# Kernel tuning notes

Hardware: AMD Instinct MI355X
Metric: run time of the kernel (lower is better)

Reference implementation:

```python
import jax, jax.numpy as jnp
import numpy as np

B, S, D, H, E, K = 4, 2048, 768, 3072, 8, 2
LB_SCALE = 0.01
NOISY_STD = 1.0


def setup_inputs() -> dict:
    key = jax.random.key(0)
    ks = jax.random.split(key, 8)
    x = jax.random.normal(ks[0], (B, S, D), jnp.float32)
    # gate_linear: nn.Linear(D, E, bias=False); torch weight is [E, D]
    gate_w = jax.random.normal(ks[1], (E, D), jnp.float32) * 0.02
    noise_weight = jnp.zeros((E,), jnp.float32)  # initialized to zeros in torch
    noise = jax.random.normal(ks[2], (B, S, E), jnp.float32)  # torch.randn_like(logits)
    # expert weights stored in (in, out) layout: y = x @ w + b
    w1 = jax.random.normal(ks[3], (E, D, H), jnp.float32) * 0.02
    b1 = jnp.zeros((E, H), jnp.float32)
    w2 = jax.random.normal(ks[4], (E, D, H), jnp.float32) * 0.02
    b2 = jnp.zeros((E, H), jnp.float32)
    wp = jax.random.normal(ks[5], (E, H, D), jnp.float32) * 0.02
    bp = jnp.zeros((E, D), jnp.float32)
    return {"x": x, "gate_w": gate_w, "noise_weight": noise_weight, "noise": noise,
            "w1": w1, "b1": b1, "w2": w2, "b2": b2, "wp": wp, "bp": bp}


def reference(x, gate_w, noise_weight, noise, w1, b1, w2, b2, wp, bp):
    num_experts = gate_w.shape[0]
    # --- TopKGateParallel ---
    logits = jnp.einsum('bsd,ed->bse', x, gate_w)            # [B,S,E]
    gate_weights = jax.nn.softmax(logits, axis=-1)
    gate_weights_mean = gate_weights.reshape(-1, num_experts).mean(0)
    uniform = 1.0 / num_experts
    load_balance_loss = jnp.mean((gate_weights_mean - uniform) ** 2) * LB_SCALE
    logits_noisy = logits + noise * NOISY_STD * noise_weight  # noise_weight zeros => no-op at init
    top_k_vals, top_k_ids = jax.lax.top_k(logits_noisy, K)    # [B,S,K]
    # scatter top-k back into a -inf tensor, then softmax -> sparse gates
    topk_mask = jax.nn.one_hot(top_k_ids, num_experts, dtype=logits.dtype).sum(-2) > 0  # [B,S,E]
    sparse_logits = jnp.where(topk_mask, logits_noisy, -jnp.inf)
    gates = jax.nn.softmax(sparse_logits, axis=-1)            # zeros outside top-k
    # --- per-expert SwiGLU, weighted combine (gates are exactly 0 off top-k) ---
    y = jnp.zeros_like(x)
    for e in range(num_experts):  # small fixed expert count
        h = (x @ w1[e] + b1[e]) * jax.nn.silu(x @ w2[e] + b2[e])  # [B,S,H]
        y = y + gates[..., e:e + 1] * (h @ wp[e] + bp[e])
    return y, load_balance_loss
```

## Files before the change

kernel.cpp:

```cpp
#include <hip/hip_runtime.h>
#include <hip/hip_bf16.h>

#define NTOK 8192
#define DDIM 768
#define HDIM 3072
#define NEXP 8
#define MROWS (NTOK*2)

typedef float f32x4 __attribute__((ext_vector_type(4)));
typedef short bf16x8 __attribute__((ext_vector_type(8)));
typedef unsigned short u16x4 __attribute__((ext_vector_type(4)));

__device__ __forceinline__ unsigned short f2bf(float f) {
  union { float f; unsigned u; } v; v.f = f;
  unsigned r = v.u + 0x7fffu + ((v.u >> 16) & 1u);
  return (unsigned short)(r >> 16);
}

typedef __attribute__((address_space(3))) unsigned int* lds_ptr_t;
typedef const __attribute__((address_space(1))) unsigned int* gbl_ptr_t;
__device__ __forceinline__ void async16(const void* g, void* l) {
  __builtin_amdgcn_global_load_lds((gbl_ptr_t)g, (lds_ptr_t)l, 16, 0, 0);
}

__global__ __launch_bounds__(128) void gating_kernel(
    const float* __restrict__ x, const float* __restrict__ gw,
    const float* __restrict__ nw, const float* __restrict__ noise,
    int* counts, float* sums, int* tok_list, float* gate_list,
    int* tok_top, float* gate_top)
{
  __shared__ float s_gw[NEXP*DDIM];
  __shared__ float s_sums[NEXP];
  __shared__ float s_nw[NEXP];
  int tid = threadIdx.x;
  for (int i = tid; i < NEXP*DDIM/4; i += 128)
    ((f32x4*)s_gw)[i] = ((const f32x4*)gw)[i];
  if (tid < NEXP) { s_sums[tid] = 0.f; s_nw[tid] = nw[tid]; }
  __syncthreads();
  int t = blockIdx.x*128 + tid;
  float acc[NEXP];
  #pragma unroll
  for (int e = 0; e < NEXP; ++e) acc[e] = 0.f;
  const f32x4* xr = (const f32x4*)(x + (size_t)t*DDIM);
  for (int d4 = 0; d4 < DDIM/4; ++d4) {
    f32x4 xv = xr[d4];
    #pragma unroll
    for (int e = 0; e < NEXP; ++e) {
      f32x4 g = *(const f32x4*)&s_gw[e*DDIM + d4*4];
      acc[e] += xv.x*g.x + xv.y*g.y + xv.z*g.z + xv.w*g.w;
    }
  }
  float m = acc[0];
  #pragma unroll
  for (int e = 1; e < NEXP; ++e) m = fmaxf(m, acc[e]);
  float p[NEXP], s = 0.f;
  #pragma unroll
  for (int e = 0; e < NEXP; ++e) { p[e] = __expf(acc[e]-m); s += p[e]; }
  float inv = 1.f/s;
  #pragma unroll
  for (int e = 0; e < NEXP; ++e) atomicAdd(&s_sums[e], p[e]*inv);
  float ln[NEXP];
  #pragma unroll
  for (int e = 0; e < NEXP; ++e) ln[e] = acc[e] + noise[(size_t)t*NEXP+e]*s_nw[e];
  int i0 = 0; float v0 = ln[0];
  #pragma unroll
  for (int e = 1; e < NEXP; ++e) if (ln[e] > v0) { v0 = ln[e]; i0 = e; }
  int i1 = -1; float v1 = 0.f;
  #pragma unroll
  for (int e = 0; e < NEXP; ++e)
    if (e != i0 && (i1 < 0 || ln[e] > v1)) { v1 = ln[e]; i1 = e; }
  float e1 = __expf(v1 - v0);
  float g0 = 1.f/(1.f + e1);
  float g1 = e1*g0;
  int p0 = atomicAdd(&counts[i0], 1);
  tok_list[i0*NTOK + p0] = t; gate_list[i0*NTOK + p0] = g0;
  int p1 = atomicAdd(&counts[i1], 1);
  tok_list[i1*NTOK + p1] = t; gate_list[i1*NTOK + p1] = g1;
  tok_top[2*t] = i0; tok_top[2*t+1] = i1;
  gate_top[2*t] = g0; gate_top[2*t+1] = g1;
  __syncthreads();
  if (tid < NEXP) atomicAdd(&sums[tid], s_sums[tid]);
}

__global__ void finalize_kernel(const int* counts, const float* sums,
                                int* offsets, float* loss_out)
{
  if (threadIdx.x == 0) {
    int o = 0;
    #pragma unroll
    for (int e = 0; e < NEXP; ++e) { offsets[e] = o; o += counts[e]; }
    offsets[NEXP] = o;
    float l = 0.f;
    #pragma unroll
    for (int e = 0; e < NEXP; ++e) {
      float dv = sums[e]*(1.f/(float)NTOK) - 1.f/(float)NEXP;
      l += dv*dv;
    }
    loss_out[0] = l*(0.01f/(float)NEXP);
  }
}

__global__ __launch_bounds__(256) void cvt_x_kernel(const float* __restrict__ x,
                                                    unsigned short* __restrict__ xb)
{
  int i = blockIdx.x*256 + threadIdx.x;
  f32x4 v = ((const f32x4*)x)[i];
  u16x4 o; o.x = f2bf(v.x); o.y = f2bf(v.y); o.z = f2bf(v.z); o.w = f2bf(v.w);
  ((u16x4*)xb)[i] = o;
}

__global__ __launch_bounds__(256) void transpose_cvt_kernel(
    const float* __restrict__ src, unsigned short* __restrict__ dst, int R, int C)
{
  __shared__ unsigned short s[64*65];
  int e = blockIdx.z;
  int r0 = blockIdx.y*64, c0 = blockIdx.x*64;
  const float* sp = src + ((size_t)e*R + r0)*C + c0;
  unsigned short* dp = dst + ((size_t)e*C + c0)*R + r0;
  int t = threadIdx.x;
  #pragma unroll
  for (int i = 0; i < 16; ++i) {
    int idx = t + 256*i;
    int r = idx >> 6, c = idx & 63;
    s[c*65 + r] = f2bf(sp[(size_t)r*C + c]);
  }
  __syncthreads();
  #pragma unroll
  for (int i = 0; i < 16; ++i) {
    int idx = t + 256*i;
    int c = idx >> 6, r = idx & 63;
    dp[(size_t)c*R + r] = s[c*65 + r];
  }
}

__global__ __launch_bounds__(256) void compact_kernel(
    const int* __restrict__ counts, const int* __restrict__ offsets,
    const int* __restrict__ tok_list, const float* __restrict__ gate_list,
    int* __restrict__ row_token, float* __restrict__ row_gate)
{
  int e = blockIdx.y;
  int pos = blockIdx.x*256 + threadIdx.x;
  if (pos < counts[e]) {
    int r = offsets[e] + pos;
    row_token[r] = tok_list[e*NTOK + pos];
    row_gate[r]  = gate_list[e*NTOK + pos];
  }
}

__global__ __launch_bounds__(256) void init_y_kernel(
    const int* __restrict__ tok_top, const float* __restrict__ gate_top,
    const float* __restrict__ bp, float* __restrict__ y)
{
  int i = blockIdx.x*256 + threadIdx.x;
  int t = i / (DDIM/4);
  int d4 = i % (DDIM/4);
  int e0 = tok_top[2*t], e1 = tok_top[2*t+1];
  float g0 = gate_top[2*t], g1 = gate_top[2*t+1];
  f32x4 b0 = ((const f32x4*)(bp + (size_t)e0*DDIM))[d4];
  f32x4 b1v = ((const f32x4*)(bp + (size_t)e1*DDIM))[d4];
  ((f32x4*)y)[i] = g0*b0 + g1*b1v;
}

__global__ __launch_bounds__(256) void ffn1_mfma(
    const unsigned short* __restrict__ xb,
    const unsigned short* __restrict__ w1T, const unsigned short* __restrict__ w2T,
    const float* __restrict__ b1, const float* __restrict__ b2,
    const int* __restrict__ offsets, const int* __restrict__ row_token,
    unsigned short* __restrict__ h_buf, int h_base, int HC)
{
  int e = blockIdx.z;
  int r_lo = offsets[e];
  int rows_e = offsets[e+1] - r_lo;
  int bx = blockIdx.x;
  if (bx*128 >= rows_e) return;
  int r0 = r_lo + bx*128;
  int rows_valid = rows_e - bx*128; if (rows_valid > 128) rows_valid = 128;
  int h0 = h_base + blockIdx.y*64;

  __shared__ __align__(16) char sL[16384];
  __shared__ int s_tok[128];

  int tid = threadIdx.x;
  if (tid < 128) {
    int r = r0 + tid; if (r > MROWS-1) r = MROWS-1;
    s_tok[tid] = row_token[r];
  }
  __syncthreads();
  int lane = tid & 63, wc = tid >> 6;
  int l4r = lane >> 2, l4c = lane & 3;
  int quad = lane >> 4, l16 = lane & 15;

  const unsigned short* gA0 = xb + (size_t)s_tok[wc*16 + l4r]*DDIM + l4c*8;
  const unsigned short* gA1 = xb + (size_t)s_tok[(wc+4)*16 + l4r]*DDIM + l4c*8;
  const unsigned short* gB1 = w1T + ((size_t)e*HDIM + h0 + wc*16 + l4r)*DDIM + l4c*8;
  const unsigned short* gB2 = w2T + ((size_t)e*HDIM + h0 + wc*16 + l4r)*DDIM + l4c*8;
  char* lA0 = sL + wc*1024;
  char* lA1 = sL + (wc+4)*1024;
  char* lB1 = sL + 8192 + wc*1024;
  char* lB2 = sL + 12288 + wc*1024;

  f32x4 acc1[8], acc2[8];
  #pragma unroll
  for (int i = 0; i < 8; ++i) { acc1[i] = (f32x4){0,0,0,0}; acc2[i] = (f32x4){0,0,0,0}; }

  for (int k0 = 0; k0 < DDIM; k0 += 32) {
    async16(gA0 + k0, lA0);
    async16(gA1 + k0, lA1);
    async16(gB1 + k0, lB1);
    async16(gB2 + k0, lB2);
    __syncthreads();
    bf16x8 bf1 = *(const bf16x8*)(sL + 8192 + (wc*16 + l16)*64 + quad*16);
    bf16x8 bf2 = *(const bf16x8*)(sL + 12288 + (wc*16 + l16)*64 + quad*16);
    #pragma unroll
    for (int mt = 0; mt < 8; ++mt) {
      bf16x8 af = *(const bf16x8*)(sL + (mt*16 + l16)*64 + quad*16);
      acc1[mt] = __builtin_amdgcn_mfma_f32_16x16x32_bf16(af, bf1, acc1[mt], 0, 0, 0);
      acc2[mt] = __builtin_amdgcn_mfma_f32_16x16x32_bf16(af, bf2, acc2[mt], 0, 0, 0);
    }
    __syncthreads();
  }
  int hcol = h0 + wc*16 + l16;
  float bb1 = b1[(size_t)e*HDIM + hcol];
  float bb2 = b2[(size_t)e*HDIM + hcol];
  int hl = hcol - h_base;
  #pragma unroll
  for (int mt = 0; mt < 8; ++mt) {
    #pragma unroll
    for (int r = 0; r < 4; ++r) {
      int row = mt*16 + quad*4 + r;
      if (row < rows_valid) {
        float c1 = acc1[mt][r] + bb1;
        float c2 = acc2[mt][r] + bb2;
        float hv = c1 * (c2 / (1.f + __expf(-c2)));
        h_buf[(size_t)(r0 + row)*HC + hl] = f2bf(hv);
      }
    }
  }
}

__global__ __launch_bounds__(256) void ffn2_mfma(
    const unsigned short* __restrict__ h_buf, const unsigned short* __restrict__ wpT,
    const int* __restrict__ offsets, const int* __restrict__ row_token,
    const float* __restrict__ row_gate, float* __restrict__ y, int h_base, int HC)
{
  int e = blockIdx.z;
  int r_lo = offsets[e];
  int rows_e = offsets[e+1] - r_lo;
  int bx = blockIdx.x;
  if (bx*128 >= rows_e) return;
  int r0 = r_lo + bx*128;
  int rows_valid = rows_e - bx*128; if (rows_valid > 128) rows_valid = 128;
  int c0 = blockIdx.y*128;

  __shared__ __align__(16) char sL[16384];
  __shared__ int s_tok[128];
  __shared__ float s_gate[128];

  int tid = threadIdx.x;
  if (tid < 128) {
    int r = r0 + tid; if (r > MROWS-1) r = MROWS-1;
    s_tok[tid]  = row_token[r];
    s_gate[tid] = row_gate[r];
  }
  int lane = tid & 63, wc = tid >> 6;
  int l4r = lane >> 2, l4c = lane & 3;
  int quad = lane >> 4, l16 = lane & 15;

  int rA0 = r0 + wc*16 + l4r;     if (rA0 > MROWS-1) rA0 = MROWS-1;
  int rA1 = r0 + (wc+4)*16 + l4r; if (rA1 > MROWS-1) rA1 = MROWS-1;
  const unsigned short* gA0 = h_buf + (size_t)rA0*HC + l4c*8;
  const unsigned short* gA1 = h_buf + (size_t)rA1*HC + l4c*8;
  const unsigned short* gB0 = wpT + ((size_t)e*DDIM + c0 + wc*16 + l4r)*HDIM + h_base + l4c*8;
  const unsigned short* gB1 = wpT + ((size_t)e*DDIM + c0 + (wc+4)*16 + l4r)*HDIM + h_base + l4c*8;
  char* lA0 = sL + wc*1024;
  char* lA1 = sL + (wc+4)*1024;
  char* lB0 = sL + 8192 + wc*1024;
  char* lB1 = sL + 8192 + (wc+4)*1024;

  f32x4 acc[8][2];
  #pragma unroll
  for (int i = 0; i < 8; ++i) { acc[i][0] = (f32x4){0,0,0,0}; acc[i][1] = (f32x4){0,0,0,0}; }
  __syncthreads();

  for (int k0 = 0; k0 < HC; k0 += 32) {
    async16(gA0 + k0, lA0);
    async16(gA1 + k0, lA1);
    async16(gB0 + k0, lB0);
    async16(gB1 + k0, lB1);
    __syncthreads();
    bf16x8 bfr0 = *(const bf16x8*)(sL + 8192 + (wc*32 + l16)*64 + quad*16);
    bf16x8 bfr1 = *(const bf16x8*)(sL + 8192 + (wc*32 + 16 + l16)*64 + quad*16);
    #pragma unroll
    for (int mt = 0; mt < 8; ++mt) {
      bf16x8 af = *(const bf16x8*)(sL + (mt*16 + l16)*64 + quad*16);
      acc[mt][0] = __builtin_amdgcn_mfma_f32_16x16x32_bf16(af, bfr0, acc[mt][0], 0, 0, 0);
      acc[mt][1] = __builtin_amdgcn_mfma_f32_16x16x32_bf16(af, bfr1, acc[mt][1], 0, 0, 0);
    }
    __syncthreads();
  }
  #pragma unroll
  for (int nt = 0; nt < 2; ++nt) {
    int col = c0 + wc*32 + nt*16 + l16;
    #pragma unroll
    for (int mt = 0; mt < 8; ++mt) {
      #pragma unroll
      for (int r = 0; r < 4; ++r) {
        int row = mt*16 + quad*4 + r;
        if (row < rows_valid)
          atomicAdd(&y[(size_t)s_tok[row]*DDIM + col], s_gate[row]*acc[mt][nt][r]);
      }
    }
  }
}

__global__ __launch_bounds__(256) void ffn2_kernel(
    const unsigned short* __restrict__ h_buf, const float* __restrict__ wp,
    const int* __restrict__ offsets, const int* __restrict__ row_token,
    const float* __restrict__ row_gate, float* __restrict__ y, int h_base, int HC)
{
  int e = blockIdx.z;
  int r_lo = offsets[e];
  int rows_e = offsets[e+1] - r_lo;
  int bx = blockIdx.x;
  if (bx*128 >= rows_e) return;
  int r0 = r_lo + bx*128;
  int rows_valid = rows_e - bx*128; if (rows_valid > 128) rows_valid = 128;
  int c0 = blockIdx.y*128;

  __shared__ unsigned short sA[128*40];
  __shared__ int s_tok[128];
  __shared__ float s_gate[128];

  int tid = threadIdx.x;
  if (tid < 128) {
    int r = r0 + tid; if (r > MROWS-1) r = MROWS-1;
    s_tok[tid]  = row_token[r];
    s_gate[tid] = row_gate[r];
  }
  int lane = tid & 63;
  int wc = tid >> 6;
  int quad = lane >> 4, l16 = lane & 15;

  const float* wp0 = wp + (size_t)e*HDIM*DDIM + c0 + wc*32 + l16;

  f32x4 acc[8][2];
  #pragma unroll
  for (int i = 0; i < 8; ++i) { acc[i][0] = (f32x4){0,0,0,0}; acc[i][1] = (f32x4){0,0,0,0}; }
  __syncthreads();

  for (int k0 = 0; k0 < HC; k0 += 32) {
    #pragma unroll
    for (int i = 0; i < 2; ++i) {
      int c = i*256 + tid;
      int row = c >> 2, k8 = c & 3;
      int rr = r0 + row; if (rr > MROWS-1) rr = MROWS-1;
      bf16x8 v = *(const bf16x8*)(h_buf + (size_t)rr*HC + k0 + k8*8);
      *(bf16x8*)&sA[row*40 + k8*8] = v;
    }
    float bv[2][8];
    #pragma unroll
    for (int nt = 0; nt < 2; ++nt)
      #pragma unroll
      for (int j = 0; j < 8; ++j)
        bv[nt][j] = wp0[(size_t)(h_base + k0 + quad*8 + j)*DDIM + nt*16];
    bf16x8 bfr[2];
    #pragma unroll
    for (int nt = 0; nt < 2; ++nt)
      #pragma unroll
      for (int j = 0; j < 8; ++j) bfr[nt][j] = (short)f2bf(bv[nt][j]);
    __syncthreads();
    #pragma unroll
    for (int mt = 0; mt < 8; ++mt) {
      bf16x8 af = *(const bf16x8*)&sA[(mt*16 + l16)*40 + quad*8];
      acc[mt][0] = __builtin_amdgcn_mfma_f32_16x16x32_bf16(af, bfr[0], acc[mt][0], 0, 0, 0);
      acc[mt][1] = __builtin_amdgcn_mfma_f32_16x16x32_bf16(af, bfr[1], acc[mt][1], 0, 0, 0);
    }
    __syncthreads();
  }
  #pragma unroll
  for (int nt = 0; nt < 2; ++nt) {
    int col = c0 + wc*32 + nt*16 + l16;
    #pragma unroll
    for (int mt = 0; mt < 8; ++mt) {
      #pragma unroll
      for (int r = 0; r < 4; ++r) {
        int row = mt*16 + quad*4 + r;
        if (row < rows_valid)
          atomicAdd(&y[(size_t)s_tok[row]*DDIM + col], s_gate[row]*acc[mt][nt][r]);
      }
    }
  }
}

extern "C" void kernel_launch(void* const* d_in, const int* in_sizes, int n_in,
                              void* d_out, int out_size, void* d_ws, size_t ws_size,
                              hipStream_t stream)
{
  (void)in_sizes; (void)n_in; (void)out_size;
  const float* x     = (const float*)d_in[0];
  const float* gw    = (const float*)d_in[1];
  const float* nw    = (const float*)d_in[2];
  const float* noise = (const float*)d_in[3];
  const float* w1    = (const float*)d_in[4];
  const float* b1    = (const float*)d_in[5];
  const float* w2    = (const float*)d_in[6];
  const float* b2    = (const float*)d_in[7];
  const float* wp    = (const float*)d_in[8];
  const float* bp    = (const float*)d_in[9];
  float* y = (float*)d_out;

  char* ws = (char*)d_ws;
  int*   counts   = (int*)(ws + 0);
  float* sums     = (float*)(ws + 64);
  int*   offsets  = (int*)(ws + 128);
  size_t off = 256;
  int*   tok_list  = (int*)(ws + off);   off += (size_t)NEXP*NTOK*4;
  float* gate_list = (float*)(ws + off); off += (size_t)NEXP*NTOK*4;
  int*   tok_top   = (int*)(ws + off);   off += (size_t)NTOK*2*4;
  float* gate_top  = (float*)(ws + off); off += (size_t)NTOK*2*4;
  int*   row_token = (int*)(ws + off);   off += (size_t)MROWS*4;
  float* row_gate  = (float*)(ws + off); off += (size_t)MROWS*4;
  unsigned short* xb = (unsigned short*)(ws + off); off += (size_t)NTOK*DDIM*2;

  const size_t WT = (size_t)NEXP*DDIM*HDIM*2;
  unsigned short* w1T = (unsigned short*)(ws + off);
  unsigned short* w2T = (unsigned short*)(ws + off + WT);
  unsigned short* wpT = (unsigned short*)(ws + off + 2*WT);
  bool haveP = (off + 3*WT + (size_t)MROWS*64*2 <= ws_size);
  size_t oH = off + (haveP ? 3*WT : 2*WT);

  static const int hc_opts[6] = {3072, 1536, 768, 384, 192, 64};
  int HC = 64;
  for (int i = 0; i < 6; ++i)
    if (oH + (size_t)MROWS*hc_opts[i]*2 <= ws_size) { HC = hc_opts[i]; break; }
  unsigned short* h_buf = (unsigned short*)(ws + oH);

  hipMemsetAsync(d_ws, 0, 256, stream);
  gating_kernel<<<NTOK/128, 128, 0, stream>>>(x, gw, nw, noise, counts, sums,
                                              tok_list, gate_list, tok_top, gate_top);
  finalize_kernel<<<1, 64, 0, stream>>>(counts, sums, offsets, y + (size_t)NTOK*DDIM);
  cvt_x_kernel<<<NTOK*DDIM/1024, 256, 0, stream>>>(x, xb);
  compact_kernel<<<dim3(NTOK/256, NEXP), 256, 0, stream>>>(counts, offsets, tok_list,
                                                           gate_list, row_token, row_gate);
  init_y_kernel<<<NTOK*DDIM/1024, 256, 0, stream>>>(tok_top, gate_top, bp, y);

  transpose_cvt_kernel<<<dim3(HDIM/64, DDIM/64, NEXP), 256, 0, stream>>>(w1, w1T, DDIM, HDIM);
  transpose_cvt_kernel<<<dim3(HDIM/64, DDIM/64, NEXP), 256, 0, stream>>>(w2, w2T, DDIM, HDIM);
  if (haveP)
    transpose_cvt_kernel<<<dim3(DDIM/64, HDIM/64, NEXP), 256, 0, stream>>>(wp, wpT, HDIM, DDIM);

  int nch = HDIM / HC;
  for (int c = 0; c < nch; ++c) {
    ffn1_mfma<<<dim3(64, HC/64, NEXP), 256, 0, stream>>>(xb, w1T, w2T, b1, b2, offsets,
                                                         row_token, h_buf, c*HC, HC);
    if (haveP)
      ffn2_mfma<<<dim3(64, DDIM/128, NEXP), 256, 0, stream>>>(h_buf, wpT, offsets, row_token,
                                                              row_gate, y, c*HC, HC);
    else
      ffn2_kernel<<<dim3(64, DDIM/128, NEXP), 256, 0, stream>>>(h_buf, wp, offsets, row_token,
                                                                row_gate, y, c*HC, HC);
  }
}
```

Baseline: 999.3 us.

## Enlarge MoE GEMM tiles and XOR-swizzle LDS layout in ffn1/ffn2

ffn1 now uses 512-thread blocks computing 256x128 tiles for both w1 and w2, and ffn2 computes 256x128 tiles with 4x8 MFMA subtiles per wave. This raises MFMA work per LDS load and cuts redundant reloads of the weight and activation tiles. The LDS layout is XOR-swizzled on the 16-byte k segment to reduce bank conflicts on fragment reads. The minimum h chunk size and the grids are adjusted to match. The trade-offs are more registers per thread, fewer blocks when few tokens are routed to an expert, and more padding waste on ragged tiles.

Result: slower. 1.725 ms (+72.6%).

```diff
diff --git a/kernel.cpp b/kernel.cpp
--- a/kernel.cpp
+++ b/kernel.cpp
@@ -161,7 +161,7 @@
   ((f32x4*)y)[i] = g0*b0 + g1*b1v;
 }
 
-__global__ __launch_bounds__(256) void ffn1_mfma(
+__global__ __launch_bounds__(512, 2) void ffn1_mfma(
     const unsigned short* __restrict__ xb,
     const unsigned short* __restrict__ w1T, const unsigned short* __restrict__ w2T,
     const float* __restrict__ b1, const float* __restrict__ b2,
@@ -172,36 +172,46 @@
   int r_lo = offsets[e];
   int rows_e = offsets[e+1] - r_lo;
   int bx = blockIdx.x;
-  if (bx*128 >= rows_e) return;
-  int r0 = r_lo + bx*128;
-  int rows_valid = rows_e - bx*128; if (rows_valid > 128) rows_valid = 128;
-  int h0 = h_base + blockIdx.y*64;
-
-  __shared__ __align__(16) char sL[16384];
-  __shared__ int s_tok[128];
+  if (bx*256 >= rows_e) return;
+  int r0 = r_lo + bx*256;
+  int rows_valid = rows_e - bx*256; if (rows_valid > 256) rows_valid = 256;
+  int h0 = h_base + blockIdx.y*128;
+
+  __shared__ __align__(16) char sA[16384];
+  __shared__ __align__(16) char sB[16384];
+  __shared__ int s_tok[256];
 
   int tid = threadIdx.x;
-  if (tid < 128) {
+  if (tid < 256) {
     int r = r0 + tid; if (r > MROWS-1) r = MROWS-1;
     s_tok[tid] = row_token[r];
   }
   __syncthreads();
-  int lane = tid & 63, wc = tid >> 6;
-  int l4r = lane >> 2, l4c = lane & 3;
-  int quad = lane >> 4, l16 = lane & 15;
-
-  const unsigned short* gA0 = xb + (size_t)s_tok[wc*16 + l4r]*DDIM + l4c*8;
-  const unsigned short* gA1 = xb + (size_t)s_tok[(wc+4)*16 + l4r]*DDIM + l4c*8;
-  const unsigned short* gB1 = w1T + ((size_t)e*HDIM + h0 + wc*16 + l4r)*DDIM + l4c*8;
-  const unsigned short* gB2 = w2T + ((size_t)e*HDIM + h0 + wc*16 + l4r)*DDIM + l4c*8;
-  char* lA0 = sL + wc*1024;
-  char* lA1 = sL + (wc+4)*1024;
-  char* lB1 = sL + 8192 + wc*1024;
-  char* lB2 = sL + 12288 + wc*1024;
-
-  f32x4 acc1[8], acc2[8];
-  #pragma unroll
-  for (int i = 0; i < 8; ++i) { acc1[i] = (f32x4){0,0,0,0}; acc2[i] = (f32x4){0,0,0,0}; }
+
+  int lane = tid & 63, w = tid >> 6;
+  int wr = w & 3, wcg = w >> 2;
+  int l16 = lane & 15, quad = lane >> 4;
+  int lr = lane >> 2, ls = lane & 3;
+  int kseg = ls ^ (lr & 3);
+
+  const unsigned short* gA0 = xb + (size_t)s_tok[w*16 + lr]*DDIM + kseg*8;
+  const unsigned short* gA1 = xb + (size_t)s_tok[(8+w)*16 + lr]*DDIM + kseg*8;
+  const unsigned short* gB1 = w1T + ((size_t)e*HDIM + h0 + w*16 + lr)*DDIM + kseg*8;
+  const unsigned short* gB2 = w2T + ((size_t)e*HDIM + h0 + w*16 + lr)*DDIM + kseg*8;
+  char* lA0 = sA + w*1024;
+  char* lA1 = sA + (8+w)*1024;
+  char* lB1 = sB + w*1024;
+  char* lB2 = sB + (8+w)*1024;
+
+  f32x4 acc[2][4][4];
+  #pragma unroll
+  for (int m = 0; m < 2; ++m)
+    #pragma unroll
+    for (int i = 0; i < 4; ++i)
+      #pragma unroll
+      for (int j = 0; j < 4; ++j) acc[m][i][j] = (f32x4){0,0,0,0};
+
+  int swz = (quad ^ (l16 & 3))*16 + l16*64;
 
   for (int k0 = 0; k0 < DDIM; k0 += 32) {
     async16(gA0 + k0, lA0);
@@ -209,36 +219,46 @@
     async16(gB1 + k0, lB1);
     async16(gB2 + k0, lB2);
     __syncthreads();
-    bf16x8 bf1 = *(const bf16x8*)(sL + 8192 + (wc*16 + l16)*64 + quad*16);
-    bf16x8 bf2 = *(const bf16x8*)(sL + 12288 + (wc*16 + l16)*64 + quad*16);
-    #pragma unroll
-    for (int mt = 0; mt < 8; ++mt) {
-      bf16x8 af = *(const bf16x8*)(sL + (mt*16 + l16)*64 + quad*16);
-      acc1[mt] = __builtin_amdgcn_mfma_f32_16x16x32_bf16(af, bf1, acc1[mt], 0, 0, 0);
-      acc2[mt] = __builtin_amdgcn_mfma_f32_16x16x32_bf16(af, bf2, acc2[mt], 0, 0, 0);
-    }
-    __syncthreads();
-  }
-  int hcol = h0 + wc*16 + l16;
-  float bb1 = b1[(size_t)e*HDIM + hcol];
-  float bb2 = b2[(size_t)e*HDIM + hcol];
-  int hl = hcol - h_base;
-  #pragma unroll
-  for (int mt = 0; mt < 8; ++mt) {
-    #pragma unroll
-    for (int r = 0; r < 4; ++r) {
-      int row = mt*16 + quad*4 + r;
-      if (row < rows_valid) {
-        float c1 = acc1[mt][r] + bb1;
-        float c2 = acc2[mt][r] + bb2;
-        float hv = c1 * (c2 / (1.f + __expf(-c2)));
-        h_buf[(size_t)(r0 + row)*HC + hl] = f2bf(hv);
+    bf16x8 bfr[2][4];
+    #pragma unroll
+    for (int m = 0; m < 2; ++m)
+      #pragma unroll
+      for (int nt = 0; nt < 4; ++nt)
+        bfr[m][nt] = *(const bf16x8*)(sB + (m*8 + wcg*4 + nt)*1024 + swz);
+    #pragma unroll
+    for (int mt = 0; mt < 4; ++mt) {
+      bf16x8 af = *(const bf16x8*)(sA + (wr*4 + mt)*1024 + swz);
+      #pragma unroll
+      for (int m = 0; m < 2; ++m)
+        #pragma unroll
+        for (int nt = 0; nt < 4; ++nt)
+          acc[m][mt][nt] = __builtin_amdgcn_mfma_f32_16x16x32_bf16(af, bfr[m][nt], acc[m][mt][nt], 0, 0, 0);
+    }
+    __syncthreads();
+  }
+  #pragma unroll
+  for (int nt = 0; nt < 4; ++nt) {
+    int col = h0 + wcg*64 + nt*16 + l16;
+    float bb1 = b1[(size_t)e*HDIM + col];
+    float bb2 = b2[(size_t)e*HDIM + col];
+    int cl = col - h_base;
+    #pragma unroll
+    for (int mt = 0; mt < 4; ++mt) {
+      #pragma unroll
+      for (int r = 0; r < 4; ++r) {
+        int row = wr*64 + mt*16 + quad*4 + r;
+        if (row < rows_valid) {
+          float c1 = acc[0][mt][nt][r] + bb1;
+          float c2 = acc[1][mt][nt][r] + bb2;
+          float hv = c1 * (c2 / (1.f + __expf(-c2)));
+          h_buf[(size_t)(r0 + row)*HC + cl] = f2bf(hv);
+        }
       }
     }
   }
 }
 
-__global__ __launch_bounds__(256) void ffn2_mfma(
+__global__ __launch_bounds__(256, 2) void ffn2_mfma(
     const unsigned short* __restrict__ h_buf, const unsigned short* __restrict__ wpT,
     const int* __restrict__ offsets, const int* __restrict__ row_token,
     const float* __restrict__ row_gate, float* __restrict__ y, int h_base, int HC)
@@ -247,65 +267,75 @@
   int r_lo = offsets[e];
   int rows_e = offsets[e+1] - r_lo;
   int bx = blockIdx.x;
-  if (bx*128 >= rows_e) return;
-  int r0 = r_lo + bx*128;
-  int rows_valid = rows_e - bx*128; if (rows_valid > 128) rows_valid = 128;
+  if (bx*256 >= rows_e) return;
+  int r0 = r_lo + bx*256;
+  int rows_valid = rows_e - bx*256; if (rows_valid > 256) rows_valid = 256;
   int c0 = blockIdx.y*128;
 
-  __shared__ __align__(16) char sL[16384];
-  __shared__ int s_tok[128];
-  __shared__ float s_gate[128];
+  __shared__ __align__(16) char sA[16384];
+  __shared__ __align__(16) char sB[8192];
+  __shared__ int s_tok[256];
+  __shared__ float s_gate[256];
 
   int tid = threadIdx.x;
-  if (tid < 128) {
+  {
     int r = r0 + tid; if (r > MROWS-1) r = MROWS-1;
     s_tok[tid]  = row_token[r];
     s_gate[tid] = row_gate[r];
   }
-  int lane = tid & 63, wc = tid >> 6;
-  int l4r = lane >> 2, l4c = lane & 3;
-  int quad = lane >> 4, l16 = lane & 15;
-
-  int rA0 = r0 + wc*16 + l4r;     if (rA0 > MROWS-1) rA0 = MROWS-1;
-  int rA1 = r0 + (wc+4)*16 + l4r; if (rA1 > MROWS-1) rA1 = MROWS-1;
-  const unsigned short* gA0 = h_buf + (size_t)rA0*HC + l4c*8;
-  const unsigned short* gA1 = h_buf + (size_t)rA1*HC + l4c*8;
-  const unsigned short* gB0 = wpT + ((size_t)e*DDIM + c0 + wc*16 + l4r)*HDIM + h_base + l4c*8;
-  const unsigned short* gB1 = wpT + ((size_t)e*DDIM + c0 + (wc+4)*16 + l4r)*HDIM + h_base + l4c*8;
-  char* lA0 = sL + wc*1024;
-  char* lA1 = sL + (wc+4)*1024;
-  char* lB0 = sL + 8192 + wc*1024;
-  char* lB1 = sL + 8192 + (wc+4)*1024;
-
-  f32x4 acc[8][2];
-  #pragma unroll
-  for (int i = 0; i < 8; ++i) { acc[i][0] = (f32x4){0,0,0,0}; acc[i][1] = (f32x4){0,0,0,0}; }
-  __syncthreads();
+  __syncthreads();
+
+  int lane = tid & 63, w = tid >> 6;
+  int l16 = lane & 15, quad = lane >> 4;
+  int lr = lane >> 2, ls = lane & 3;
+  int kseg = ls ^ (lr & 3);
+
+  const unsigned short* gA[4];
+  #pragma unroll
+  for (int i = 0; i < 4; ++i) {
+    int rr = r0 + (i*4 + w)*16 + lr; if (rr > MROWS-1) rr = MROWS-1;
+    gA[i] = h_buf + (size_t)rr*HC + kseg*8;
+  }
+  const unsigned short* gB[2];
+  #pragma unroll
+  for (int i = 0; i < 2; ++i)
+    gB[i] = wpT + ((size_t)e*DDIM + c0 + (i*4 + w)*16 + lr)*HDIM + h_base + kseg*8;
+
+  f32x4 acc[4][8];
+  #pragma unroll
+  for (int i = 0; i < 4; ++i)
+    #pragma unroll
+    for (int j = 0; j < 8; ++j) acc[i][j] = (f32x4){0,0,0,0};
+
+  int swz = (quad ^ (l16 & 3))*16 + l16*64;
 
   for (int k0 = 0; k0 < HC; k0 += 32) {
-    async16(gA0 + k0, lA0);
-    async16(gA1 + k0, lA1);
-    async16(gB0 + k0, lB0);
-    async16(gB1 + k0, lB1);
-    __syncthreads();
-    bf16x8 bfr0 = *(const bf16x8*)(sL + 8192 + (wc*32 + l16)*64 + quad*16);
-    bf16x8 bfr1 = *(const bf16x8*)(sL + 8192 + (wc*32 + 16 + l16)*64 + quad*16);
-    #pragma unroll
-    for (int mt = 0; mt < 8; ++mt) {
-      bf16x8 af = *(const bf16x8*)(sL + (mt*16 + l16)*64 + quad*16);
-      acc[mt][0] = __builtin_amdgcn_mfma_f32_16x16x32_bf16(af, bfr0, acc[mt][0], 0, 0, 0);
-      acc[mt][1] = __builtin_amdgcn_mfma_f32_16x16x32_bf16(af, bfr1, acc[mt][1], 0, 0, 0);
-    }
-    __syncthreads();
-  }
-  #pragma unroll
-  for (int nt = 0; nt < 2; ++nt) {
-    int col = c0 + wc*32 + nt*16 + l16;
-    #pragma unroll
-    for (int mt = 0; mt < 8; ++mt) {
+    #pragma unroll
+    for (int i = 0; i < 4; ++i) async16(gA[i] + k0, sA + ((i*4 + w)*1024) + 0*(size_t)lane);
+    #pragma unroll
+    for (int i = 0; i < 2; ++i) async16(gB[i] + k0, sB + ((i*4 + w)*1024));
+    __syncthreads();
+    bf16x8 bfr[8];
+    #pragma unroll
+    for (int nt = 0; nt < 8; ++nt)
+      bfr[nt] = *(const bf16x8*)(sB + nt*1024 + swz);
+    #pragma unroll
+    for (int mt = 0; mt < 4; ++mt) {
+      bf16x8 af = *(const bf16x8*)(sA + (w*4 + mt)*1024 + swz);
+      #pragma unroll
+      for (int nt = 0; nt < 8; ++nt)
+        acc[mt][nt] = __builtin_amdgcn_mfma_f32_16x16x32_bf16(af, bfr[nt], acc[mt][nt], 0, 0, 0);
+    }
+    __syncthreads();
+  }
+  #pragma unroll
+  for (int nt = 0; nt < 8; ++nt) {
+    int col = c0 + nt*16 + l16;
+    #pragma unroll
+    for (int mt = 0; mt < 4; ++mt) {
       #pragma unroll
       for (int r = 0; r < 4; ++r) {
-        int row = mt*16 + quad*4 + r;
+        int row = w*64 + mt*16 + quad*4 + r;
         if (row < rows_valid)
           atomicAdd(&y[(size_t)s_tok[row]*DDIM + col], s_gate[row]*acc[mt][nt][r]);
       }
@@ -426,11 +456,11 @@
   unsigned short* w1T = (unsigned short*)(ws + off);
   unsigned short* w2T = (unsigned short*)(ws + off + WT);
   unsigned short* wpT = (unsigned short*)(ws + off + 2*WT);
-  bool haveP = (off + 3*WT + (size_t)MROWS*64*2 <= ws_size);
+  bool haveP = (off + 3*WT + (size_t)MROWS*128*2 <= ws_size);
   size_t oH = off + (haveP ? 3*WT : 2*WT);
 
-  static const int hc_opts[6] = {3072, 1536, 768, 384, 192, 64};
-  int HC = 64;
+  static const int hc_opts[6] = {3072, 1536, 768, 384, 256, 128};
+  int HC = 128;
   for (int i = 0; i < 6; ++i)
     if (oH + (size_t)MROWS*hc_opts[i]*2 <= ws_size) { HC = hc_opts[i]; break; }
   unsigned short* h_buf = (unsigned short*)(ws + oH);
@@ -451,10 +481,10 @@
 
   int nch = HDIM / HC;
   for (int c = 0; c < nch; ++c) {
-    ffn1_mfma<<<dim3(64, HC/64, NEXP), 256, 0, stream>>>(xb, w1T, w2T, b1, b2, offsets,
-                                                         row_token, h_buf, c*HC, HC);
+    ffn1_mfma<<<dim3(32, HC/128, NEXP), 512, 0, stream>>>(xb, w1T, w2T, b1, b2, offsets,
+                                                          row_token, h_buf, c*HC, HC);
     if (haveP)
-      ffn2_mfma<<<dim3(64, DDIM/128, NEXP), 256, 0, stream>>>(h_buf, wpT, offsets, row_token,
+      ffn2_mfma<<<dim3(32, DDIM/128, NEXP), 256, 0, stream>>>(h_buf, wpT, offsets, row_token,
                                                               row_gate, y, c*HC, HC);
     else
       ffn2_kernel<<<dim3(64, DDIM/128, NEXP), 256, 0, stream>>>(h_buf, wp, offsets, row_token,
```

## Deepen MFMA K-tiles, square ffn2 warp tiles, replace atomic combine with gather pass

Applied to the files above, without the earlier changes.

Both expert GEMM kernels now stage 64-wide K slices per barrier instead of 32, which halves the number of sync rounds. ffn2 switches to a 2x2 warp layout with 4x4 accumulator tiles so each warp reuses its A and B fragments more. When the workspace is large enough, the full hidden buffer is computed in one pass. ffn2 then writes per-row partial outputs, and a new combine kernel gathers the two expert results per token with gates and biases, which avoids float atomics into y. Other changes: the w1/w2 transposes are merged into one launch and the grid x dimension is doubled. These cost extra workspace and one more full read and write of the partial buffer.

After: 1.006 ms. No clear change (+0.7%).

```diff
diff --git a/kernel.cpp b/kernel.cpp
--- a/kernel.cpp
+++ b/kernel.cpp
@@ -27,7 +27,7 @@
     const float* __restrict__ x, const float* __restrict__ gw,
     const float* __restrict__ nw, const float* __restrict__ noise,
     int* counts, float* sums, int* tok_list, float* gate_list,
-    int* tok_top, float* gate_top)
+    int* tok_top, float* gate_top, int* pos_top)
 {
   __shared__ float s_gw[NEXP*DDIM];
   __shared__ float s_sums[NEXP];
@@ -78,6 +78,7 @@
   tok_list[i1*NTOK + p1] = t; gate_list[i1*NTOK + p1] = g1;
   tok_top[2*t] = i0; tok_top[2*t+1] = i1;
   gate_top[2*t] = g0; gate_top[2*t+1] = g1;
+  pos_top[2*t] = p0; pos_top[2*t+1] = p1;
   __syncthreads();
   if (tid < NEXP) atomicAdd(&sums[tid], s_sums[tid]);
 }
@@ -107,6 +108,35 @@
   f32x4 v = ((const f32x4*)x)[i];
   u16x4 o; o.x = f2bf(v.x); o.y = f2bf(v.y); o.z = f2bf(v.z); o.w = f2bf(v.w);
   ((u16x4*)xb)[i] = o;
+}
+
+__global__ __launch_bounds__(256) void transpose_cvt2_kernel(
+    const float* __restrict__ src1, unsigned short* __restrict__ dst1,
+    const float* __restrict__ src2, unsigned short* __restrict__ dst2,
+    int R, int C)
+{
+  __shared__ unsigned short s[64*65];
+  int z = blockIdx.z;
+  int e = z & (NEXP-1);
+  const float* src = (z < NEXP) ? src1 : src2;
+  unsigned short* dst = (z < NEXP) ? dst1 : dst2;
+  int r0 = blockIdx.y*64, c0 = blockIdx.x*64;
+  const float* sp = src + ((size_t)e*R + r0)*C + c0;
+  unsigned short* dp = dst + ((size_t)e*C + c0)*R + r0;
+  int t = threadIdx.x;
+  #pragma unroll
+  for (int i = 0; i < 16; ++i) {
+    int idx = t + 256*i;
+    int r = idx >> 6, c = idx & 63;
+    s[c*65 + r] = f2bf(sp[(size_t)r*C + c]);
+  }
+  __syncthreads();
+  #pragma unroll
+  for (int i = 0; i < 16; ++i) {
+    int idx = t + 256*i;
+    int c = idx >> 6, r = idx & 63;
+    dp[(size_t)c*R + r] = s[c*65 + r];
+  }
 }
 
 __global__ __launch_bounds__(256) void transpose_cvt_kernel(
@@ -177,7 +207,8 @@
   int rows_valid = rows_e - bx*128; if (rows_valid > 128) rows_valid = 128;
   int h0 = h_base + blockIdx.y*64;
 
-  __shared__ __align__(16) char sL[16384];
+  __shared__ __align__(16) char sA[16384];
+  __shared__ __align__(16) char sB[16384];
   __shared__ int s_tok[128];
 
   int tid = threadIdx.x;
@@ -186,40 +217,52 @@
     s_tok[tid] = row_token[r];
   }
   __syncthreads();
-  int lane = tid & 63, wc = tid >> 6;
-  int l4r = lane >> 2, l4c = lane & 3;
-  int quad = lane >> 4, l16 = lane & 15;
-
-  const unsigned short* gA0 = xb + (size_t)s_tok[wc*16 + l4r]*DDIM + l4c*8;
-  const unsigned short* gA1 = xb + (size_t)s_tok[(wc+4)*16 + l4r]*DDIM + l4c*8;
-  const unsigned short* gB1 = w1T + ((size_t)e*HDIM + h0 + wc*16 + l4r)*DDIM + l4c*8;
-  const unsigned short* gB2 = w2T + ((size_t)e*HDIM + h0 + wc*16 + l4r)*DDIM + l4c*8;
-  char* lA0 = sL + wc*1024;
-  char* lA1 = sL + (wc+4)*1024;
-  char* lB1 = sL + 8192 + wc*1024;
-  char* lB2 = sL + 12288 + wc*1024;
+
+  int lane = tid & 63, w = tid >> 6;
+  int l16 = lane & 15, quad = lane >> 4;
+  int lr = lane >> 2, ls = lane & 3;
+
+  const unsigned short* gA[4]; char* lA[4];
+  const unsigned short* gB[4]; char* lB[4];
+  #pragma unroll
+  for (int i = 0; i < 4; ++i) {
+    int slot = i*4 + w;
+    int chunk = slot & 7, kh = slot >> 3;
+    gA[i] = xb + (size_t)s_tok[chunk*16 + lr]*DDIM + kh*32 + ls*8;
+    lA[i] = sA + slot*1024;
+    int mat = (slot >> 2) & 1;
+    int col = h0 + w*16 + lr;
+    const unsigned short* base = mat ? w2T : w1T;
+    gB[i] = base + ((size_t)e*HDIM + col)*DDIM + kh*32 + ls*8;
+    lB[i] = sB + slot*1024;
+  }
 
   f32x4 acc1[8], acc2[8];
   #pragma unroll
   for (int i = 0; i < 8; ++i) { acc1[i] = (f32x4){0,0,0,0}; acc2[i] = (f32x4){0,0,0,0}; }
 
-  for (int k0 = 0; k0 < DDIM; k0 += 32) {
-    async16(gA0 + k0, lA0);
-    async16(gA1 + k0, lA1);
-    async16(gB1 + k0, lB1);
-    async16(gB2 + k0, lB2);
+  int fro = l16*64 + quad*16;
+
+  for (int k0 = 0; k0 < DDIM; k0 += 64) {
+    #pragma unroll
+    for (int i = 0; i < 4; ++i) async16(gA[i] + k0, lA[i]);
+    #pragma unroll
+    for (int i = 0; i < 4; ++i) async16(gB[i] + k0, lB[i]);
     __syncthreads();
-    bf16x8 bf1 = *(const bf16x8*)(sL + 8192 + (wc*16 + l16)*64 + quad*16);
-    bf16x8 bf2 = *(const bf16x8*)(sL + 12288 + (wc*16 + l16)*64 + quad*16);
-    #pragma unroll
-    for (int mt = 0; mt < 8; ++mt) {
-      bf16x8 af = *(const bf16x8*)(sL + (mt*16 + l16)*64 + quad*16);
-      acc1[mt] = __builtin_amdgcn_mfma_f32_16x16x32_bf16(af, bf1, acc1[mt], 0, 0, 0);
-      acc2[mt] = __builtin_amdgcn_mfma_f32_16x16x32_bf16(af, bf2, acc2[mt], 0, 0, 0);
+    #pragma unroll
+    for (int kh = 0; kh < 2; ++kh) {
+      bf16x8 bf1 = *(const bf16x8*)(sB + (kh*8 + w)*1024 + fro);
+      bf16x8 bf2 = *(const bf16x8*)(sB + (kh*8 + 4 + w)*1024 + fro);
+      #pragma unroll
+      for (int mt = 0; mt < 8; ++mt) {
+        bf16x8 af = *(const bf16x8*)(sA + (kh*8 + mt)*1024 + fro);
+        acc1[mt] = __builtin_amdgcn_mfma_f32_16x16x32_bf16(af, bf1, acc1[mt], 0, 0, 0);
+        acc2[mt] = __builtin_amdgcn_mfma_f32_16x16x32_bf16(af, bf2, acc2[mt], 0, 0, 0);
+      }
     }
     __syncthreads();
   }
-  int hcol = h0 + wc*16 + l16;
+  int hcol = h0 + w*16 + l16;
   float bb1 = b1[(size_t)e*HDIM + hcol];
   float bb2 = b2[(size_t)e*HDIM + hcol];
   int hl = hcol - h_base;
@@ -241,7 +284,8 @@
 __global__ __launch_bounds__(256) void ffn2_mfma(
     const unsigned short* __restrict__ h_buf, const unsigned short* __restrict__ wpT,
     const int* __restrict__ offsets, const int* __restrict__ row_token,
-    const float* __restrict__ row_gate, float* __restrict__ y, int h_base, int HC)
+    const float* __restrict__ row_gate, float* __restrict__ outp,
+    int h_base, int HC, int mode)
 {
   int e = blockIdx.z;
   int r_lo = offsets[e];
@@ -252,7 +296,8 @@
   int rows_valid = rows_e - bx*128; if (rows_valid > 128) rows_valid = 128;
   int c0 = blockIdx.y*128;
 
-  __shared__ __align__(16) char sL[16384];
+  __shared__ __align__(16) char sA[16384];
+  __shared__ __align__(16) char sB[16384];
   __shared__ int s_tok[128];
   __shared__ float s_gate[128];
 
@@ -262,55 +307,107 @@
     s_tok[tid]  = row_token[r];
     s_gate[tid] = row_gate[r];
   }
-  int lane = tid & 63, wc = tid >> 6;
-  int l4r = lane >> 2, l4c = lane & 3;
-  int quad = lane >> 4, l16 = lane & 15;
-
-  int rA0 = r0 + wc*16 + l4r;     if (rA0 > MROWS-1) rA0 = MROWS-1;
-  int rA1 = r0 + (wc+4)*16 + l4r; if (rA1 > MROWS-1) rA1 = MROWS-1;
-  const unsigned short* gA0 = h_buf + (size_t)rA0*HC + l4c*8;
-  const unsigned short* gA1 = h_buf + (size_t)rA1*HC + l4c*8;
-  const unsigned short* gB0 = wpT + ((size_t)e*DDIM + c0 + wc*16 + l4r)*HDIM + h_base + l4c*8;
-  const unsigned short* gB1 = wpT + ((size_t)e*DDIM + c0 + (wc+4)*16 + l4r)*HDIM + h_base + l4c*8;
-  char* lA0 = sL + wc*1024;
-  char* lA1 = sL + (wc+4)*1024;
-  char* lB0 = sL + 8192 + wc*1024;
-  char* lB1 = sL + 8192 + (wc+4)*1024;
-
-  f32x4 acc[8][2];
-  #pragma unroll
-  for (int i = 0; i < 8; ++i) { acc[i][0] = (f32x4){0,0,0,0}; acc[i][1] = (f32x4){0,0,0,0}; }
-  __syncthreads();
-
-  for (int k0 = 0; k0 < HC; k0 += 32) {
-    async16(gA0 + k0, lA0);
-    async16(gA1 + k0, lA1);
-    async16(gB0 + k0, lB0);
-    async16(gB1 + k0, lB1);
+  __syncthreads();
+
+  int lane = tid & 63, w = tid >> 6;
+  int l16 = lane & 15, quad = lane >> 4;
+  int lr = lane >> 2, ls = lane & 3;
+  int wr = w & 1, wcg = w >> 1;
+
+  const unsigned short* gA[4]; char* lA[4];
+  const unsigned short* gB[4]; char* lB[4];
+  #pragma unroll
+  for (int i = 0; i < 4; ++i) {
+    int slot = i*4 + w;
+    int chunk = slot & 7, kh = slot >> 3;
+    int rr = r0 + chunk*16 + lr; if (rr > MROWS-1) rr = MROWS-1;
+    gA[i] = h_buf + (size_t)rr*HC + kh*32 + ls*8;
+    lA[i] = sA + slot*1024;
+    int col = c0 + chunk*16 + lr;
+    gB[i] = wpT + ((size_t)e*DDIM + col)*HDIM + h_base + kh*32 + ls*8;
+    lB[i] = sB + slot*1024;
+  }
+
+  f32x4 acc[4][4];
+  #pragma unroll
+  for (int i = 0; i < 4; ++i)
+    #pragma unroll
+    for (int j = 0; j < 4; ++j) acc[i][j] = (f32x4){0,0,0,0};
+
+  int fro = l16*64 + quad*16;
+
+  for (int k0 = 0; k0 < HC; k0 += 64) {
+    #pragma unroll
+    for (int i = 0; i < 4; ++i) async16(gA[i] + k0, lA[i]);
+    #pragma unroll
+    for (int i = 0; i < 4; ++i) async16(gB[i] + k0, lB[i]);
     __syncthreads();
-    bf16x8 bfr0 = *(const bf16x8*)(sL + 8192 + (wc*32 + l16)*64 + quad*16);
-    bf16x8 bfr1 = *(const bf16x8*)(sL + 8192 + (wc*32 + 16 + l16)*64 + quad*16);
-    #pragma unroll
-    for (int mt = 0; mt < 8; ++mt) {
-      bf16x8 af = *(const bf16x8*)(sL + (mt*16 + l16)*64 + quad*16);
-      acc[mt][0] = __builtin_amdgcn_mfma_f32_16x16x32_bf16(af, bfr0, acc[mt][0], 0, 0, 0);
-      acc[mt][1] = __builtin_amdgcn_mfma_f32_16x16x32_bf16(af, bfr1, acc[mt][1], 0, 0, 0);
+    #pragma unroll
+    for (int kh = 0; kh < 2; ++kh) {
+      bf16x8 bfr[4];
+      #pragma unroll
+      for (int nt = 0; nt < 4; ++nt)
+        bfr[nt] = *(const bf16x8*)(sB + (kh*8 + wcg*4 + nt)*1024 + fro);
+      #pragma unroll
+      for (int mt = 0; mt < 4; ++mt) {
+        bf16x8 af = *(const bf16x8*)(sA + (kh*8 + wr*4 + mt)*1024 + fro);
+        #pragma unroll
+        for (int nt = 0; nt < 4; ++nt)
+          acc[mt][nt] = __builtin_amdgcn_mfma_f32_16x16x32_bf16(af, bfr[nt], acc[mt][nt], 0, 0, 0);
+      }
     }
     __syncthreads();
   }
-  #pragma unroll
-  for (int nt = 0; nt < 2; ++nt) {
-    int col = c0 + wc*32 + nt*16 + l16;
-    #pragma unroll
-    for (int mt = 0; mt < 8; ++mt) {
-      #pragma unroll
-      for (int r = 0; r < 4; ++r) {
-        int row = mt*16 + quad*4 + r;
-        if (row < rows_valid)
-          atomicAdd(&y[(size_t)s_tok[row]*DDIM + col], s_gate[row]*acc[mt][nt][r]);
+
+  if (mode == 0) {
+    #pragma unroll
+    for (int nt = 0; nt < 4; ++nt) {
+      int col = c0 + wcg*64 + nt*16 + l16;
+      #pragma unroll
+      for (int mt = 0; mt < 4; ++mt) {
+        #pragma unroll
+        for (int r = 0; r < 4; ++r) {
+          int row = wr*64 + mt*16 + quad*4 + r;
+          if (row < rows_valid)
+            outp[(size_t)(r0 + row)*DDIM + col] = acc[mt][nt][r];
+        }
       }
     }
-  }
+  } else {
+    #pragma unroll
+    for (int nt = 0; nt < 4; ++nt) {
+      int col = c0 + wcg*64 + nt*16 + l16;
+      #pragma unroll
+      for (int mt = 0; mt < 4; ++mt) {
+        #pragma unroll
+        for (int r = 0; r < 4; ++r) {
+          int row = wr*64 + mt*16 + quad*4 + r;
+          if (row < rows_valid)
+            atomicAdd(&outp[(size_t)s_tok[row]*DDIM + col], s_gate[row]*acc[mt][nt][r]);
+        }
+      }
+    }
+  }
+}
+
+__global__ __launch_bounds__(256) void combine_kernel(
+    const float* __restrict__ part, const int* __restrict__ tok_top,
+    const float* __restrict__ gate_top, const int* __restrict__ pos_top,
+    const int* __restrict__ offsets, const float* __restrict__ bp,
+    float* __restrict__ y)
+{
+  int i = blockIdx.x*256 + threadIdx.x;
+  int t = i / (DDIM/4);
+  int d4 = i % (DDIM/4);
+  int e0 = tok_top[2*t], e1 = tok_top[2*t+1];
+  float g0 = gate_top[2*t], g1 = gate_top[2*t+1];
+  int r0 = offsets[e0] + pos_top[2*t];
+  int r1 = offsets[e1] + pos_top[2*t+1];
+  f32x4 v0 = ((const f32x4*)part)[(size_t)r0*(DDIM/4) + d4];
+  f32x4 v1 = ((const f32x4*)part)[(size_t)r1*(DDIM/4) + d4];
+  f32x4 b0 = ((const f32x4*)(bp + (size_t)e0*DDIM))[d4];
+  f32x4 b1v = ((const f32x4*)(bp + (size_t)e1*DDIM))[d4];
+  ((f32x4*)y)[i] = g0*(v0 + b0) + g1*(v1 + b1v);
 }
 
 __global__ __launch_bounds__(256) void ffn2_kernel(
@@ -418,46 +515,70 @@
   float* gate_list = (float*)(ws + off); off += (size_t)NEXP*NTOK*4;
   int*   tok_top   = (int*)(ws + off);   off += (size_t)NTOK*2*4;
   float* gate_top  = (float*)(ws + off); off += (size_t)NTOK*2*4;
+  int*   pos_top   = (int*)(ws + off);   off += (size_t)NTOK*2*4;
   int*   row_token = (int*)(ws + off);   off += (size_t)MROWS*4;
   float* row_gate  = (float*)(ws + off); off += (size_t)MROWS*4;
   unsigned short* xb = (unsigned short*)(ws + off); off += (size_t)NTOK*DDIM*2;
 
-  const size_t WT = (size_t)NEXP*DDIM*HDIM*2;
+  const size_t WT    = (size_t)NEXP*DDIM*HDIM*2;
+  const size_t HFULL = (size_t)MROWS*HDIM*2;
+  const size_t PSZ   = (size_t)MROWS*DDIM*4;
+
   unsigned short* w1T = (unsigned short*)(ws + off);
   unsigned short* w2T = (unsigned short*)(ws + off + WT);
   unsigned short* wpT = (unsigned short*)(ws + off + 2*WT);
-  bool haveP = (off + 3*WT + (size_t)MROWS*64*2 <= ws_size);
+
+  bool tierA = (off + 3*WT + HFULL + PSZ <= ws_size);
+  bool haveP = (off + 3*WT + (size_t)MROWS*128*2 <= ws_size);
   size_t oH = off + (haveP ? 3*WT : 2*WT);
 
-  static const int hc_opts[6] = {3072, 1536, 768, 384, 192, 64};
-  int HC = 64;
-  for (int i = 0; i < 6; ++i)
-    if (oH + (size_t)MROWS*hc_opts[i]*2 <= ws_size) { HC = hc_opts[i]; break; }
-  unsigned short* h_buf = (unsigned short*)(ws + oH);
+  int HC;
+  unsigned short* h_buf;
+  float* part = nullptr;
+  if (tierA) {
+    HC = HDIM;
+    h_buf = (unsigned short*)(ws + off + 3*WT);
+    part  = (float*)(ws + off + 3*WT + HFULL);
+  } else {
+    static const int hc_opts[6] = {3072, 1536, 768, 384, 192, 128};
+    HC = 128;
+    for (int i = 0; i < 6; ++i)
+      if (oH + (size_t)MROWS*hc_opts[i]*2 <= ws_size) { HC = hc_opts[i]; break; }
+    h_buf = (unsigned short*)(ws + oH);
+  }
 
   hipMemsetAsync(d_ws, 0, 256, stream);
+  cvt_x_kernel<<<NTOK*DDIM/1024, 256, 0, stream>>>(x, xb);
+  transpose_cvt2_kernel<<<dim3(HDIM/64, DDIM/64, NEXP*2), 256, 0, stream>>>(
+      w1, w1T, w2, w2T, DDIM, HDIM);
+  if (haveP)
+    transpose_cvt_kernel<<<dim3(DDIM/64, HDIM/64, NEXP), 256, 0, stream>>>(wp, wpT, HDIM, DDIM);
+
   gating_kernel<<<NTOK/128, 128, 0, stream>>>(x, gw, nw, noise, counts, sums,
-                                              tok_list, gate_list, tok_top, gate_top);
+                                              tok_list, gate_list, tok_top, gate_top, pos_top);
   finalize_kernel<<<1, 64, 0, stream>>>(counts, sums, offsets, y + (size_t)NTOK*DDIM);
-  cvt_x_kernel<<<NTOK*DDIM/1024, 256, 0, stream>>>(x, xb);
   compact_kernel<<<dim3(NTOK/256, NEXP), 256, 0, stream>>>(counts, offsets, tok_list,
                                                            gate_list, row_token, row_gate);
-  init_y_kernel<<<NTOK*DDIM/1024, 256, 0, stream>>>(tok_top, gate_top, bp, y);
-
-  transpose_cvt_kernel<<<dim3(HDIM/64, DDIM/64, NEXP), 256, 0, stream>>>(w1, w1T, DDIM, HDIM);
-  transpose_cvt_kernel<<<dim3(HDIM/64, DDIM/64, NEXP), 256, 0, stream>>>(w2, w2T, DDIM, HDIM);
-  if (haveP)
-    transpose_cvt_kernel<<<dim3(DDIM/64, HDIM/64, NEXP), 256, 0, stream>>>(wp, wpT, HDIM, DDIM);
-
-  int nch = HDIM / HC;
-  for (int c = 0; c < nch; ++c) {
-    ffn1_mfma<<<dim3(64, HC/64, NEXP), 256, 0, stream>>>(xb, w1T, w2T, b1, b2, offsets,
-                                                         row_token, h_buf, c*HC, HC);
-    if (haveP)
-      ffn2_mfma<<<dim3(64, DDIM/128, NEXP), 256, 0, stream>>>(h_buf, wpT, offsets, row_token,
-                                                              row_gate, y, c*HC, HC);
-    else
-      ffn2_kernel<<<dim3(64, DDIM/128, NEXP), 256, 0, stream>>>(h_buf, wp, offsets, row_token,
-                                                                row_gate, y, c*HC, HC);
-  }
-}
+
+  if (tierA) {
+    ffn1_mfma<<<dim3(128, HDIM/64, NEXP), 256, 0, stream>>>(xb, w1T, w2T, b1, b2, offsets,
+                                                            row_token, h_buf, 0, HC);
+    ffn2_mfma<<<dim3(128, DDIM/128, NEXP), 256, 0, stream>>>(h_buf, wpT, offsets, row_token,
+                                                             row_gate, part, 0, HC, 0);
+    combine_kernel<<<NTOK*DDIM/1024, 256, 0, stream>>>(part, tok_top, gate_top, pos_top,
+                                                       offsets, bp, y);
+  } else {
+    init_y_kernel<<<NTOK*DDIM/1024, 256, 0, stream>>>(tok_top, gate_top, bp, y);
+    int nch = HDIM / HC;
+    for (int c = 0; c < nch; ++c) {
+      ffn1_mfma<<<dim3(128, HC/64, NEXP), 256, 0, stream>>>(xb, w1T, w2T, b1, b2, offsets,
+                                                            row_token, h_buf, c*HC, HC);
+      if (haveP)
+        ffn2_mfma<<<dim3(128, DDIM/128, NEXP), 256, 0, stream>>>(h_buf, wpT, offsets, row_token,
+                                                                 row_gate, y, c*HC, HC, 1);
+      else
+        ffn2_kernel<<<dim3(128, DDIM/128, NEXP), 256, 0, stream>>>(h_buf, wp, offsets, row_token,
+                                                                   row_gate, y, c*HC, HC);
+    }
+  }
+}
```
